# Kernel optimization log

Hardware: AMD Instinct MI355X
Metric: run time of the kernel (lower is better)

## Reference

```python
import jax, jax.numpy as jnp
import numpy as np

HEADS = 4
C_HEAD = 32


def setup_inputs() -> dict:
    key = jax.random.key(0)
    k1, k2, k3 = jax.random.split(key, 3)
    c_in = 256
    c_hid = HEADS * C_HEAD  # 128
    x = jax.random.normal(k1, (4, c_in, 64, 64), dtype=jnp.float32)
    # 1x1 conv weights stored as [out, in]
    w_qkv = jax.random.normal(k2, (3 * c_hid, c_in), dtype=jnp.float32) * (c_in ** -0.5)
    w_out = jax.random.normal(k3, (c_in, c_hid), dtype=jnp.float32) * (c_hid ** -0.5)
    b_out = jnp.zeros((c_in,), dtype=jnp.float32)
    return {"x": x, "w_qkv": w_qkv, "w_out": w_out, "b_out": b_out}


def reference(x, w_qkv, w_out, b_out):
    b, c, h, w = x.shape
    scale = C_HEAD ** -0.5
    # 1x1 conv == channel matmul
    qkv = jnp.einsum('bchw,oc->bohw', x, w_qkv)  # [b, 3*c_hid, h, w]
    q, k, v = jnp.split(qkv, 3, axis=1)
    # b (heads c_head) x y -> b heads c_head (x y)
    def to_heads(t):
        return t.reshape(b, HEADS, C_HEAD, h * w)
    q, k, v = to_heads(q) * scale, to_heads(k), to_heads(v)
    sim = jnp.einsum('bhci,bhcj->bhij', q, k)  # [b, heads, N, N]
    sim = sim - jax.lax.stop_gradient(jnp.max(sim, axis=-1, keepdims=True))
    attn = jax.nn.softmax(sim, axis=-1)
    out = jnp.einsum('bhij,bhcj->bhic', attn, v)  # [b, heads, N, c_head]
    # b h (x y) c -> b (h c) x y
    out = out.transpose(0, 1, 3, 2).reshape(b, HEADS * C_HEAD, h, w)
    out = jnp.einsum('bchw,oc->bohw', out, w_out) + b_out[None, :, None, None]
    return out
```

## Files before the change

kernel.cpp:

```cpp
#include <hip/hip_runtime.h>
#include <hip/hip_bf16.h>
#include <cstdint>
#include <cstddef>


#define NB 4
#define CIN 256
#define CHID 128
#define HEADS 4
#define CHEAD 32
#define NPOS 4096
#define BH 16
#define NTOT 16384
#define QKV_O 384
#define QSCALE_LOG2E 0.2550348229f

typedef float f32x2 __attribute__((ext_vector_type(2)));
typedef float f32x4 __attribute__((ext_vector_type(4)));
typedef float f32x16 __attribute__((ext_vector_type(16)));
typedef short s16x8 __attribute__((ext_vector_type(8)));

static __device__ __forceinline__ unsigned short f2bf(float f) {
    union { float f; unsigned u; } v; v.f = f;
    unsigned r = v.u + 0x7FFFu + ((v.u >> 16) & 1u);
    return (unsigned short)(r >> 16);
}

static __device__ __forceinline__ unsigned int pk2bf(float a, float b) {
    union { __hip_bfloat162 h; unsigned int u; } c;
    c.h = __float22bfloat162_rn(float2{a, b});
    return c.u;
}

static __device__ __forceinline__ void plswap(unsigned& a, unsigned& b) {
#if __has_builtin(__builtin_amdgcn_permlane32_swap)
    auto r = __builtin_amdgcn_permlane32_swap((int)a, (int)b, false, false);
    a = (unsigned)r[0];
    b = (unsigned)r[1];
#else
    int hh = (threadIdx.x >> 5) & 1;
    unsigned ta = (unsigned)__shfl_xor((int)a, 32);
    unsigned tb = (unsigned)__shfl_xor((int)b, 32);
    unsigned na = hh ? tb : a;
    unsigned nb = hh ? b : ta;
    a = na; b = nb;
#endif
}

static __device__ __forceinline__ s16x8 mk8(unsigned a, unsigned b, unsigned c, unsigned d) {
    union { unsigned u[4]; s16x8 v; } x;
    x.u[0] = a; x.u[1] = b; x.u[2] = c; x.u[3] = d;
    return x.v;
}

static __device__ __forceinline__ void async_cp16(const void* g, void* l) {
    __builtin_amdgcn_global_load_lds((const __attribute__((address_space(1))) unsigned int*)g,
                                     (__attribute__((address_space(3))) unsigned int*)l, 16, 0, 0);
}

#define MFMA32(a, b, c) __builtin_amdgcn_mfma_f32_32x32x16_bf16(a, b, c, 0, 0, 0)


#define PTILES (NB * (CIN / 64) * (NPOS / 64))
__global__ __launch_bounds__(256) void k_prep(const float* __restrict__ x,
                                              unsigned short* __restrict__ xT,
                                              const float* __restrict__ wqkv,
                                              const float* __restrict__ wout,
                                              unsigned short* __restrict__ wqkv_bf,
                                              unsigned short* __restrict__ wout_bf) {
    if (blockIdx.x >= PTILES) {
        int i = (blockIdx.x - PTILES) * 256 + threadIdx.x;
        if (i < QKV_O * CIN) wqkv_bf[i] = f2bf(wqkv[i]);
        if (i < CIN * CHID)  wout_bf[i] = f2bf(wout[i]);
        return;
    }
    __shared__ float tile[64][65];
    const int per_b = (CIN / 64) * (NPOS / 64);
    int b   = blockIdx.x / per_b;
    int rem = blockIdx.x % per_b;
    int ct = rem / (NPOS / 64);
    int nt = rem % (NPOS / 64);
    int c0 = ct * 64, n0 = nt * 64;
    int t = threadIdx.x;
    const float* xb = x + (size_t)b * CIN * NPOS;
#pragma unroll
    for (int it = 0; it < 4; ++it) {
        int c  = (t >> 4) + it * 16;
        int n4 = (t & 15) * 4;
        f32x4 v = *(const f32x4*)(xb + (size_t)(c0 + c) * NPOS + n0 + n4);
        tile[c][n4] = v[0]; tile[c][n4 + 1] = v[1];
        tile[c][n4 + 2] = v[2]; tile[c][n4 + 3] = v[3];
    }
    __syncthreads();
    unsigned short* xTb = xT + (size_t)b * NPOS * CIN;
#pragma unroll
    for (int it = 0; it < 2; ++it) {
        int slot = it * 256 + t;
        int n  = slot >> 3;
        int c8 = (slot & 7) * 8;
        union { unsigned short u[8]; s16x8 v; } pk;
#pragma unroll
        for (int r = 0; r < 8; ++r) pk.u[r] = f2bf(tile[c8 + r][n]);
        *(s16x8*)(xTb + (size_t)(n0 + n) * CIN + c0 + c8) = pk.v;
    }
}

__global__ __launch_bounds__(256, 4) void k_qkv(const unsigned short* __restrict__ wq,
                                                const unsigned short* __restrict__ xT,
                                                unsigned short* __restrict__ Q,
                                                unsigned short* __restrict__ K,
                                                unsigned short* __restrict__ V) {
    __shared__ __align__(16) unsigned char smem[2 * 12288];
    int mt = blockIdx.x % 3;
    int nt = blockIdx.x / 3;
    int wid = threadIdx.x >> 6, lane = threadIdx.x & 63;
    int quad = lane >> 4, low4 = lane & 15;
    int o0 = mt * 128, n0 = nt * 64;
    int lb = lane * 16;

    const unsigned short* srcA0 = wq + (size_t)(o0 + wid * 32 + low4) * CIN + quad * 8;
    const unsigned short* srcA1 = srcA0 + 16 * CIN;
    const unsigned short* srcB  = xT + (size_t)(n0 + wid * 16 + low4) * CIN + quad * 8;
    int dA0 = wid * 2048, dA1 = dA0 + 1024, dB = 8192 + wid * 1024;

    async_cp16(srcA0, smem + dA0 + lb);
    async_cp16(srcA1, smem + dA1 + lb);
    async_cp16(srcB,  smem + dB  + lb);
    __syncthreads();

    f32x4 acc[2][4] = {};
    for (int c = 0; c < 8; ++c) {
        if (c < 7) {
            unsigned char* nxt = smem + ((c + 1) & 1) * 12288;
            async_cp16(srcA0 + (c + 1) * 32, nxt + dA0 + lb);
            async_cp16(srcA1 + (c + 1) * 32, nxt + dA1 + lb);
            async_cp16(srcB  + (c + 1) * 32, nxt + dB  + lb);
        }
        const unsigned char* cur = smem + (c & 1) * 12288;
        s16x8 a0 = *(const s16x8*)(cur + wid * 2048 + lb);
        s16x8 a1 = *(const s16x8*)(cur + wid * 2048 + 1024 + lb);
#pragma unroll
        for (int j = 0; j < 4; ++j) {
            s16x8 bj = *(const s16x8*)(cur + 8192 + j * 1024 + lb);
            acc[0][j] = __builtin_amdgcn_mfma_f32_16x16x32_bf16(a0, bj, acc[0][j], 0, 0, 0);
            acc[1][j] = __builtin_amdgcn_mfma_f32_16x16x32_bf16(a1, bj, acc[1][j], 0, 0, 0);
        }
        __syncthreads();
    }

    int b = n0 >> 12, nbase = n0 & 4095;
    if (mt < 2) {
        unsigned short (*vtT)[136] = (unsigned short(*)[136])smem;
        float sc = (mt == 0) ? QSCALE_LOG2E : 1.0f;
#pragma unroll
        for (int i = 0; i < 2; ++i) {
            int ob = wid * 32 + i * 16 + quad * 4;
#pragma unroll
            for (int j = 0; j < 4; ++j) {
                int nl = j * 16 + low4;
                f32x4 v = acc[i][j];
                unsigned long long d =
                    (unsigned long long)pk2bf(v[0] * sc, v[1] * sc) |
                    ((unsigned long long)pk2bf(v[2] * sc, v[3] * sc) << 32);
                *(unsigned long long*)(&vtT[nl][ob]) = d;
            }
        }
        __syncthreads();
        if (mt == 0) {
#pragma unroll
            for (int it = 0; it < 4; ++it) {
                int slot = it * 256 + threadIdx.x;
                int n = slot >> 4, c16 = slot & 15;
                s16x8 val = *(const s16x8*)(&vtT[n][c16 * 8]);
                int o = c16 * 8, head = o >> 5, ch = o & 31;
                *(s16x8*)(Q + ((size_t)(b * 4 + head) * NPOS + nbase + n) * 32 + ch) = val;
            }
        } else {
#pragma unroll
            for (int it = 0; it < 4; ++it) {
                int slot = it * 256 + threadIdx.x;
                int c16 = slot >> 6, n = slot & 63;
                s16x8 val = *(const s16x8*)(&vtT[n][c16 * 8]);
                int o = c16 * 8, head = o >> 5, c0h = o & 31;
                int f = c0h >> 4, hh = (c0h >> 3) & 1;
                int nG = nbase + n;
                int bh = b * 4 + head;
                size_t addr = (((size_t)bh * 128 + (nG >> 5)) * 2 + f) * 512
                            + (size_t)((((hh << 5) | (nG & 31)) << 3));
                *(s16x8*)(K + addr) = val;
            }
        }
    } else {
        unsigned short* vt = (unsigned short*)smem;
#pragma unroll
        for (int i = 0; i < 2; ++i) {
            int ol = wid * 32 + i * 16 + quad * 4;
#pragma unroll
            for (int j = 0; j < 4; ++j) {
                int col = j * 16 + low4;
#pragma unroll
                for (int r = 0; r < 4; ++r) vt[(ol + r) * 80 + col] = f2bf(acc[i][j][r]);
            }
        }
        __syncthreads();
#pragma unroll
        for (int rep = 0; rep < 4; ++rep) {
            int idx = rep * 256 + threadIdx.x;
            int row = idx >> 3, c8 = idx & 7;
            s16x8 val = *(const s16x8*)(vt + row * 80 + c8 * 8);
            int head = row >> 5, ch = row & 31;
            int bh = b * 4 + head;
            int nstart = nbase + c8 * 8;
            int kc = nstart >> 4, hh = (nstart >> 3) & 1;
            *(s16x8*)(V + ((size_t)(bh * 256 + kc) * 64 + ((hh << 5) | ch)) * 8) = val;
        }
    }
}

__global__ __launch_bounds__(256, 8) void k_attn(const unsigned short* __restrict__ Q,
                                                 const unsigned short* __restrict__ K,
                                                 const unsigned short* __restrict__ V,
                                                 unsigned short* __restrict__ attnO) {
    __shared__ __align__(16) unsigned char smem[16384];
    int bh = blockIdx.x & 15;
    int qt = blockIdx.x >> 4;
    int wid = threadIdx.x >> 6;
    int lane = threadIdx.x & 63;
    int q5 = lane & 31, h = lane >> 5;
    int q0 = qt * 32;
    int k0 = wid * 1024;

    const unsigned short* Qp = Q + (size_t)bh * NPOS * 32;
    s16x8 bq0 = *(const s16x8*)(Qp + (size_t)(q0 + q5) * 32 + h * 8);
    s16x8 bq1 = *(const s16x8*)(Qp + (size_t)(q0 + q5) * 32 + 16 + h * 8);

    const unsigned short* pKf = K + (size_t)bh * 131072 + lane * 8;
    const unsigned short* pVf = V + (size_t)bh * 131072 + lane * 8;
    unsigned char* wb = smem + wid * 4096;
    const int lby = lane * 16;

    auto stage = [&](int kk) {
        const unsigned short* pk = pKf + (size_t)(kk >> 5) * 1024;
        const unsigned short* pv = pVf + (size_t)(kk >> 4) * 512;
        async_cp16(pk,       wb);
        async_cp16(pk + 512, wb + 1024);
        async_cp16(pv,       wb + 2048);
        async_cp16(pv + 512, wb + 3072);
    };

    f32x16 oT = {};
    f32x2 lacc0 = {0.0f, 0.0f}, lacc1 = {0.0f, 0.0f};

    stage(k0);

#pragma unroll 1
    for (int it = 0; it < 32; ++it) {
        asm volatile("s_waitcnt vmcnt(0)" ::: "memory");
        s16x8 ak0 = *(const s16x8*)(wb + lby);
        s16x8 ak1 = *(const s16x8*)(wb + 1024 + lby);
        s16x8 av0 = *(const s16x8*)(wb + 2048 + lby);
        s16x8 av1 = *(const s16x8*)(wb + 3072 + lby);
        asm volatile("s_waitcnt lgkmcnt(0)" ::: "memory");
        __builtin_amdgcn_sched_barrier(0);
        if (it + 1 < 32) stage(k0 + (it + 1) * 32);
        __builtin_amdgcn_sched_barrier(0);

        f32x16 s = {};
        __builtin_amdgcn_s_setprio(1);
        s = MFMA32(ak0, bq0, s);
        s = MFMA32(ak1, bq1, s);
        __builtin_amdgcn_s_setprio(0);
        unsigned p[8];
#pragma unroll
        for (int i = 0; i < 8; ++i) {
            float e0 = __builtin_amdgcn_exp2f(s[2 * i]);
            float e1 = __builtin_amdgcn_exp2f(s[2 * i + 1]);
            f32x2 e = {e0, e1};
            if (i & 1) lacc0 += e;
            else       lacc1 += e;
            p[i] = pk2bf(e0, e1);
        }
        plswap(p[0], p[2]); plswap(p[1], p[3]);
        plswap(p[4], p[6]); plswap(p[5], p[7]);
        s16x8 bplo = mk8(p[0], p[1], p[2], p[3]);
        s16x8 bphi = mk8(p[4], p[5], p[6], p[7]);
        __builtin_amdgcn_s_setprio(1);
        oT = MFMA32(av0, bplo, oT);
        oT = MFMA32(av1, bphi, oT);
        __builtin_amdgcn_s_setprio(0);
    }

    float lsum = lacc0[0] + lacc0[1] + lacc1[0] + lacc1[1];
    lsum += __shfl_xor(lsum, 32);

    __syncthreads();

    if (wid) {
        float* area = (float*)(smem + (wid - 1) * 4352);
#pragma unroll
        for (int j = 0; j < 4; ++j)
            *(f32x4*)(area + j * 256 + lane * 4) =
                f32x4{oT[4 * j], oT[4 * j + 1], oT[4 * j + 2], oT[4 * j + 3]};
        area[1024 + lane] = lsum;
    }
    __syncthreads();
    if (!wid) {
        const float* a0 = (const float*)(smem);
        const float* a1 = (const float*)(smem + 4352);
        const float* a2 = (const float*)(smem + 8704);
        lsum += a0[1024 + lane] + a1[1024 + lane] + a2[1024 + lane];
        float inv = 1.0f / lsum;
        int b = bh >> 2, head = bh & 3;
        int n = q0 + q5;
        unsigned short* base = attnO + ((size_t)(b * NPOS + n)) * CHID + head * 32 + 4 * h;
#pragma unroll
        for (int j = 0; j < 4; ++j) {
            f32x4 r0 = *(const f32x4*)(a0 + j * 256 + lane * 4);
            f32x4 r1 = *(const f32x4*)(a1 + j * 256 + lane * 4);
            f32x4 r2 = *(const f32x4*)(a2 + j * 256 + lane * 4);
            unsigned long long d =
                (unsigned long long)pk2bf((oT[4 * j] + r0[0] + r1[0] + r2[0]) * inv,
                                          (oT[4 * j + 1] + r0[1] + r1[1] + r2[1]) * inv) |
                ((unsigned long long)pk2bf((oT[4 * j + 2] + r0[2] + r1[2] + r2[2]) * inv,
                                           (oT[4 * j + 3] + r0[3] + r1[3] + r2[3]) * inv) << 32);
            *(unsigned long long*)(base + 8 * j) = d;
        }
    }
}

__global__ __launch_bounds__(256, 4) void k_out(const unsigned short* __restrict__ wo,
                                                const unsigned short* __restrict__ attnO,
                                                const float* __restrict__ bias,
                                                float* __restrict__ out) {
    __shared__ __align__(16) unsigned char smem[2 * 12288];
    int mt = blockIdx.x & 1;
    int nt = blockIdx.x >> 1;
    int wid = threadIdx.x >> 6, lane = threadIdx.x & 63;
    int quad = lane >> 4, low4 = lane & 15;
    int o0 = mt * 128, n0 = nt * 64;
    int lb = lane * 16;

    const unsigned short* srcA0 = wo + (size_t)(o0 + wid * 32 + low4) * CHID + quad * 8;
    const unsigned short* srcA1 = srcA0 + 16 * CHID;
    const unsigned short* srcB  = attnO + (size_t)(n0 + wid * 16 + low4) * CHID + quad * 8;
    int dA0 = wid * 2048, dA1 = dA0 + 1024, dB = 8192 + wid * 1024;

    async_cp16(srcA0, smem + dA0 + lb);
    async_cp16(srcA1, smem + dA1 + lb);
    async_cp16(srcB,  smem + dB  + lb);
    __syncthreads();

    f32x4 acc[2][4] = {};
    for (int c = 0; c < 4; ++c) {
        if (c < 3) {
            unsigned char* nxt = smem + ((c + 1) & 1) * 12288;
            async_cp16(srcA0 + (c + 1) * 32, nxt + dA0 + lb);
            async_cp16(srcA1 + (c + 1) * 32, nxt + dA1 + lb);
            async_cp16(srcB  + (c + 1) * 32, nxt + dB  + lb);
        }
        const unsigned char* cur = smem + (c & 1) * 12288;
        s16x8 a0 = *(const s16x8*)(cur + wid * 2048 + lb);
        s16x8 a1 = *(const s16x8*)(cur + wid * 2048 + 1024 + lb);
#pragma unroll
        for (int j = 0; j < 4; ++j) {
            s16x8 bj = *(const s16x8*)(cur + 8192 + j * 1024 + lb);
            acc[0][j] = __builtin_amdgcn_mfma_f32_16x16x32_bf16(a0, bj, acc[0][j], 0, 0, 0);
            acc[1][j] = __builtin_amdgcn_mfma_f32_16x16x32_bf16(a1, bj, acc[1][j], 0, 0, 0);
        }
        __syncthreads();
    }

    float (*larea)[68] = (float(*)[68])smem;
    int b = n0 >> 12, nb = n0 & 4095;
#pragma unroll
    for (int half = 0; half < 2; ++half) {
        if ((wid >> 1) == half) {
#pragma unroll
            for (int i = 0; i < 2; ++i) {
                int row = (wid & 1) * 32 + i * 16 + quad * 4;
                int o = o0 + half * 64 + row;
#pragma unroll
                for (int j = 0; j < 4; ++j) {
                    int nl = j * 16 + low4;
#pragma unroll
                    for (int r = 0; r < 4; ++r)
                        larea[row + r][nl] = acc[i][j][r] + bias[o + r];
                }
            }
        }
        __syncthreads();
#pragma unroll
        for (int it = 0; it < 4; ++it) {
            int slot = it * 256 + threadIdx.x;
            int row = slot >> 4, nn4 = (slot & 15) * 4;
            int o = o0 + half * 64 + row;
            f32x4 v = *(const f32x4*)(&larea[row][nn4]);
            *(f32x4*)(out + ((size_t)(b * CIN + o)) * NPOS + nb + nn4) = v;
        }
        __syncthreads();
    }
}

extern "C" void kernel_launch(void* const* d_in, const int* in_sizes, int n_in,
                              void* d_out, int out_size, void* d_ws, size_t ws_size,
                              hipStream_t stream) {
    const float* x    = (const float*)d_in[0];
    const float* wqkv = (const float*)d_in[1];
    const float* wout = (const float*)d_in[2];
    const float* bout = (const float*)d_in[3];
    float* out = (float*)d_out;

    unsigned short* Q       = (unsigned short*)d_ws;
    unsigned short* K       = Q + (size_t)BH * NPOS * 32;
    unsigned short* V       = K + (size_t)BH * NPOS * 32;
    unsigned short* attnO   = V + (size_t)BH * 32 * NPOS;
    unsigned short* xT      = attnO + (size_t)NTOT * CHID;
    unsigned short* wqkv_bf = xT + (size_t)NTOT * CIN;
    unsigned short* wout_bf = wqkv_bf + QKV_O * CIN;

    k_prep<<<PTILES + (QKV_O * CIN + 255) / 256, 256, 0, stream>>>(x, xT, wqkv, wout, wqkv_bf, wout_bf);
    k_qkv<<<3 * (NTOT / 64), 256, 0, stream>>>(wqkv_bf, xT, Q, K, V);
    k_attn<<<(NPOS / 32) * BH, 256, 0, stream>>>(Q, K, V, attnO);
    k_out<<<2 * (NTOT / 64), 256, 0, stream>>>(wout_bf, attnO, bout, out);
}
```

Measured before the change: 160.2 us.

## Compute softmax row sums via MFMA with ones and drop permlane swaps

The attention loop now gets the softmax denominator from two extra MFMAs that multiply a ones matrix by the bf16 probability tiles, replacing the per-lane VALU accumulation and the final cross-half shuffle. To avoid the permlane32 swaps, the V layout written by the projection kernel is reordered so its k-positions match the unswapped P register layout. The setprio hints and one sched_barrier are removed, and k_attn's occupancy hint drops from 8 to 4 blocks per CU. This trades VALU adds and swaps for doubled MFMA work in the inner loop, and the row sum is now taken over bf16-rounded probabilities.

Result: faster. 155.3 us (-3.1%).

```diff
diff --git a/kernel.cpp b/kernel.cpp
--- a/kernel.cpp
+++ b/kernel.cpp
@@ -30,21 +30,6 @@
     union { __hip_bfloat162 h; unsigned int u; } c;
     c.h = __float22bfloat162_rn(float2{a, b});
     return c.u;
-}
-
-static __device__ __forceinline__ void plswap(unsigned& a, unsigned& b) {
-#if __has_builtin(__builtin_amdgcn_permlane32_swap)
-    auto r = __builtin_amdgcn_permlane32_swap((int)a, (int)b, false, false);
-    a = (unsigned)r[0];
-    b = (unsigned)r[1];
-#else
-    int hh = (threadIdx.x >> 5) & 1;
-    unsigned ta = (unsigned)__shfl_xor((int)a, 32);
-    unsigned tb = (unsigned)__shfl_xor((int)b, 32);
-    unsigned na = hh ? tb : a;
-    unsigned nb = hh ? b : ta;
-    a = na; b = nb;
-#endif
 }
 
 static __device__ __forceinline__ s16x8 mk8(unsigned a, unsigned b, unsigned c, unsigned d) {
@@ -205,19 +190,23 @@
         __syncthreads();
 #pragma unroll
         for (int rep = 0; rep < 4; ++rep) {
-            int idx = rep * 256 + threadIdx.x;
-            int row = idx >> 3, c8 = idx & 7;
-            s16x8 val = *(const s16x8*)(vt + row * 80 + c8 * 8);
-            int head = row >> 5, ch = row & 31;
-            int bh = b * 4 + head;
-            int nstart = nbase + c8 * 8;
-            int kc = nstart >> 4, hh = (nstart >> 3) & 1;
-            *(s16x8*)(V + ((size_t)(bh * 256 + kc) * 64 + ((hh << 5) | ch)) * 8) = val;
-        }
-    }
-}
-
-__global__ __launch_bounds__(256, 8) void k_attn(const unsigned short* __restrict__ Q,
+            int slot = rep * 256 + threadIdx.x;
+            int head = slot >> 8;
+            int kc   = (slot >> 6) & 3;
+            int ln   = slot & 63;
+            int hi   = ln >> 5, ch = ln & 31;
+            const unsigned short* src = vt + (head * 32 + ch) * 80 + kc * 16 + 4 * hi;
+            union { unsigned long long q[2]; s16x8 v; } val;
+            val.q[0] = *(const unsigned long long*)(src);
+            val.q[1] = *(const unsigned long long*)(src + 8);
+            int bh2 = b * 4 + head;
+            int kcg = (nbase >> 4) + kc;
+            *(s16x8*)(V + ((size_t)(bh2 * 256 + kcg) * 64 + ln) * 8) = val.v;
+        }
+    }
+}
+
+__global__ __launch_bounds__(256, 4) void k_attn(const unsigned short* __restrict__ Q,
                                                  const unsigned short* __restrict__ K,
                                                  const unsigned short* __restrict__ V,
                                                  unsigned short* __restrict__ attnO) {
@@ -234,6 +223,11 @@
     s16x8 bq0 = *(const s16x8*)(Qp + (size_t)(q0 + q5) * 32 + h * 8);
     s16x8 bq1 = *(const s16x8*)(Qp + (size_t)(q0 + q5) * 32 + 16 + h * 8);
 
+    union { unsigned short u[8]; s16x8 v; } one8;
+#pragma unroll
+    for (int i = 0; i < 8; ++i) one8.u[i] = 0x3F80;
+    s16x8 aone = one8.v;
+
     const unsigned short* pKf = K + (size_t)bh * 131072 + lane * 8;
     const unsigned short* pVf = V + (size_t)bh * 131072 + lane * 8;
     unsigned char* wb = smem + wid * 4096;
@@ -249,7 +243,7 @@
     };
 
     f32x16 oT = {};
-    f32x2 lacc0 = {0.0f, 0.0f}, lacc1 = {0.0f, 0.0f};
+    f32x16 lsumT = {};
 
     stage(k0);
 
@@ -263,35 +257,24 @@
         asm volatile("s_waitcnt lgkmcnt(0)" ::: "memory");
         __builtin_amdgcn_sched_barrier(0);
         if (it + 1 < 32) stage(k0 + (it + 1) * 32);
-        __builtin_amdgcn_sched_barrier(0);
 
         f32x16 s = {};
-        __builtin_amdgcn_s_setprio(1);
         s = MFMA32(ak0, bq0, s);
         s = MFMA32(ak1, bq1, s);
-        __builtin_amdgcn_s_setprio(0);
         unsigned p[8];
 #pragma unroll
-        for (int i = 0; i < 8; ++i) {
-            float e0 = __builtin_amdgcn_exp2f(s[2 * i]);
-            float e1 = __builtin_amdgcn_exp2f(s[2 * i + 1]);
-            f32x2 e = {e0, e1};
-            if (i & 1) lacc0 += e;
-            else       lacc1 += e;
-            p[i] = pk2bf(e0, e1);
-        }
-        plswap(p[0], p[2]); plswap(p[1], p[3]);
-        plswap(p[4], p[6]); plswap(p[5], p[7]);
+        for (int i = 0; i < 8; ++i)
+            p[i] = pk2bf(__builtin_amdgcn_exp2f(s[2 * i]),
+                         __builtin_amdgcn_exp2f(s[2 * i + 1]));
         s16x8 bplo = mk8(p[0], p[1], p[2], p[3]);
         s16x8 bphi = mk8(p[4], p[5], p[6], p[7]);
-        __builtin_amdgcn_s_setprio(1);
         oT = MFMA32(av0, bplo, oT);
         oT = MFMA32(av1, bphi, oT);
-        __builtin_amdgcn_s_setprio(0);
-    }
-
-    float lsum = lacc0[0] + lacc0[1] + lacc1[0] + lacc1[1];
-    lsum += __shfl_xor(lsum, 32);
+        lsumT = MFMA32(aone, bplo, lsumT);
+        lsumT = MFMA32(aone, bphi, lsumT);
+    }
+
+    float lsum = lsumT[0];
 
     __syncthreads();
 
```
